# Kernel optimization log

Hardware: AMD Instinct MI355X
Metric: run time of the kernel (lower is better)

Reference implementation:

```python
import jax, jax.numpy as jnp
import numpy as np

# Grid derived from voxel_size=[0.2,0.2,0.2], pcr=[0,-40,-3,70.4,40,1]
NX, NY, NZ, NB = 352, 400, 20, 4


def setup_inputs() -> dict:
    key = jax.random.key(0)
    N, C = 1_000_000, 64
    kp, kb, kz, ky, kx = jax.random.split(key, 5)
    points = jax.random.normal(kp, (N, C), dtype=jnp.float32)
    b = jax.random.randint(kb, (N,), 0, NB)
    z = jax.random.randint(kz, (N,), 0, NZ)
    y = jax.random.randint(ky, (N,), 0, NY)
    x = jax.random.randint(kx, (N,), 0, NX)
    coors = jnp.stack([b, z, y, x], axis=1).astype(jnp.int32)
    return {"points": points, "coors": coors}


def reference(points, coors):
    # Dynamic scatter with mean reduction (average_points=True):
    # group points sharing the same (batch, z, y, x) voxel coordinate and
    # average their features. Padded (unused) voxel slots have coor == -1
    # and zero features, so the output shape is static ([N, C]).
    N = points.shape[0]
    b, z, y, x = coors[:, 0], coors[:, 1], coors[:, 2], coors[:, 3]
    keys = ((b.astype(jnp.int64) * NZ + z) * NY + y) * NX + x  # linearized voxel id

    uniq, inv = jnp.unique(keys, return_inverse=True, size=N, fill_value=-1)
    inv = inv.reshape(-1)

    sums = jax.ops.segment_sum(points, inv, num_segments=N)          # [N, C]
    counts = jax.ops.segment_sum(jnp.ones((N,), points.dtype), inv, num_segments=N)
    voxels = sums / jnp.maximum(counts, 1.0)[:, None]

    # decode linearized keys back to (batch, z, y, x); -1 marks padding
    valid = uniq >= 0
    ux = uniq % NX
    uy = (uniq // NX) % NY
    uz = (uniq // (NX * NY)) % NZ
    ub = uniq // (NX * NY * NZ)
    voxel_coors = jnp.stack([ub, uz, uy, ux], axis=1).astype(jnp.int32)
    voxel_coors = jnp.where(valid[:, None], voxel_coors, -1)
    return voxels, voxel_coors
```

## Files before the change

kernel.cpp:

```cpp
#include <hip/hip_runtime.h>
#include <stdint.h>

#define NXc 352
#define NYc 400
#define NZc 20
#define KS  11264000
#define WORDS 176000
#define NBLK3 688
#define NCH 64
#define RPT 4

#define OFF_A     0ull
#define OFF_P     11264000ull
#define OFF_R     12672000ull
#define OFF_BP    13376000ull
#define OFF_BC    13380096ull
#define OFF_NU    13384192ull
#define OFF_KEY   13384448ull
#define OFF_IOFF  17384448ull
#define OFF_PID   21384704ull

static __device__ __forceinline__ int keyof(int4 c) {
  return ((c.x * NZc + c.y) * NYc + c.z) * NXc + c.w;
}

__global__ void k_zero(uint4* __restrict__ A4, unsigned int m) {
  unsigned int i = blockIdx.x * 256 + threadIdx.x;
  unsigned int stride = gridDim.x * 256;
  uint4 z = make_uint4(0u, 0u, 0u, 0u);
  for (; i < m; i += stride) A4[i] = z;
}

__global__ void k_count(const int4* __restrict__ coors, unsigned int* __restrict__ A32, int n) {
  int p = blockIdx.x * 256 + threadIdx.x;
  if (p >= n) return;
  int key = keyof(coors[p]);
  atomicAdd(&A32[key >> 2], 1u << (8 * (key & 3)));
}

__global__ void k_scan1(const unsigned char* __restrict__ A,
                        unsigned int* __restrict__ bp, unsigned int* __restrict__ bc) {
  int b = blockIdx.x, t = threadIdx.x;
  int w = b * 256 + t;
  unsigned int pres = 0, cnt = 0;
  if (w < WORDS) {
    const uint4* aw = (const uint4*)(A + (size_t)w * 64);
    unsigned long long mask = 0ull;
#pragma unroll
    for (int q = 0; q < 4; q++) {
      uint4 v = aw[q];
      unsigned int us[4] = { v.x, v.y, v.z, v.w };
#pragma unroll
      for (int i = 0; i < 4; i++) {
        unsigned int u = us[i];
#pragma unroll
        for (int bb = 0; bb < 4; bb++) {
          unsigned int byte = (u >> (8 * bb)) & 0xFFu;
          cnt += byte;
          if (byte) mask |= 1ull << (q * 16 + i * 4 + bb);
        }
      }
    }
    pres = (unsigned int)__popcll(mask);
  }
  __shared__ unsigned int sp[256], sc[256];
  sp[t] = pres; sc[t] = cnt; __syncthreads();
  for (int o = 128; o > 0; o >>= 1) {
    if (t < o) { sp[t] += sp[t + o]; sc[t] += sc[t + o]; }
    __syncthreads();
  }
  if (t == 0) { bp[b] = sp[0]; bc[b] = sc[0]; }
}

__global__ void k_scan2(unsigned int* __restrict__ bp, unsigned int* __restrict__ bc,
                        unsigned int* __restrict__ nu, unsigned int* __restrict__ ioff, int n) {
  int t = threadIdx.x;
  __shared__ unsigned int sp[256], sc[256];
  unsigned int cp = 0, cc = 0;
  for (int base = 0; base < NBLK3; base += 256) {
    int i = base + t;
    unsigned int vp = (i < NBLK3) ? bp[i] : 0u;
    unsigned int vc = (i < NBLK3) ? bc[i] : 0u;
    sp[t] = vp; sc[t] = vc; __syncthreads();
    unsigned int ipv = vp, icv = vc;
    for (int o = 1; o < 256; o <<= 1) {
      unsigned int ap = (t >= o) ? sp[t - o] : 0u;
      unsigned int ac = (t >= o) ? sc[t - o] : 0u;
      __syncthreads();
      ipv += ap; icv += ac;
      sp[t] = ipv; sc[t] = icv; __syncthreads();
    }
    if (i < NBLK3) { bp[i] = cp + ipv - vp; bc[i] = cc + icv - vc; }
    unsigned int tp = sp[255], tc = sc[255];
    __syncthreads();
    cp += tp; cc += tc;
  }
  if (t == 0) { nu[0] = cp; ioff[cp] = (unsigned int)n; }
}

__global__ void k_scan3(const unsigned char* __restrict__ A,
                        const unsigned int* __restrict__ bp, const unsigned int* __restrict__ bc,
                        unsigned long long* __restrict__ P, unsigned int* __restrict__ R,
                        unsigned int* __restrict__ keyA, unsigned int* __restrict__ ioff) {
  int b = blockIdx.x, t = threadIdx.x;
  int w = b * 256 + t;
  unsigned long long mask = 0ull;
  unsigned int uu[16];
  unsigned int pres = 0, cnt = 0;
  if (w < WORDS) {
    const uint4* aw = (const uint4*)(A + (size_t)w * 64);
#pragma unroll
    for (int q = 0; q < 4; q++) {
      uint4 v = aw[q];
      uu[q * 4 + 0] = v.x; uu[q * 4 + 1] = v.y; uu[q * 4 + 2] = v.z; uu[q * 4 + 3] = v.w;
    }
#pragma unroll
    for (int i = 0; i < 16; i++) {
      unsigned int u = uu[i];
#pragma unroll
      for (int bb = 0; bb < 4; bb++) {
        unsigned int byte = (u >> (8 * bb)) & 0xFFu;
        cnt += byte;
        if (byte) mask |= 1ull << (i * 4 + bb);
      }
    }
    pres = (unsigned int)__popcll(mask);
  }
  __shared__ unsigned int sp[256], sc[256];
  sp[t] = pres; sc[t] = cnt; __syncthreads();
  unsigned int ip = pres, ic = cnt;
  for (int o = 1; o < 256; o <<= 1) {
    unsigned int ap = (t >= o) ? sp[t - o] : 0u;
    unsigned int ac = (t >= o) ? sc[t - o] : 0u;
    __syncthreads();
    ip += ap; ic += ac;
    sp[t] = ip; sc[t] = ic; __syncthreads();
  }
  if (w < WORDS) {
    unsigned int rank = bp[b] + ip - pres;
    unsigned int coff = bc[b] + ic - cnt;
    P[w] = mask; R[w] = rank;
    for (int j = 0; j < 64; j++) {
      unsigned int byte = (uu[j >> 2] >> (8 * (j & 3))) & 0xFFu;
      if (byte) {
        keyA[rank] = (unsigned int)(w * 64 + j);
        ioff[rank] = coff;
        rank++; coff += byte;
      }
    }
  }
}

__global__ void k_scatter(const int4* __restrict__ coors, unsigned int* __restrict__ A32,
                          const unsigned long long* __restrict__ P, const unsigned int* __restrict__ R,
                          const unsigned int* __restrict__ ioff, unsigned int* __restrict__ pid, int n) {
  int p = blockIdx.x * 256 + threadIdx.x;
  if (p >= n) return;
  int key = keyof(coors[p]);
  int w = key >> 6, bit = key & 63;
  unsigned long long below = (bit == 0) ? 0ull : (P[w] & ((1ull << bit) - 1ull));
  unsigned int rank = R[w] + (unsigned int)__popcll(below);
  unsigned int sh = 8u * (unsigned int)(key & 3);
  unsigned int old = atomicSub(&A32[key >> 2], 1u << sh);
  unsigned int intra = ((old >> sh) & 0xFFu) - 1u;
  pid[ioff[rank] + intra] = (unsigned int)p;
}

__global__ void k_gather(const float4* __restrict__ pts, const unsigned int* __restrict__ pid,
                         const unsigned int* __restrict__ keyA, const unsigned int* __restrict__ ioff,
                         const unsigned int* __restrict__ nu, float* __restrict__ out, int n) {
  int gt = blockIdx.x * 256 + threadIdx.x;
  int grp = gt >> 4, l = gt & 15;
  int rb = grp * RPT;
  if (rb >= n) return;
  unsigned int nU = nu[0];

  unsigned int e[RPT + 1];
#pragma unroll
  for (int j = 0; j <= RPT; j++) {
    unsigned int idx = min((unsigned int)(rb + j), nU);
    e[j] = ioff[idx];
  }

  unsigned int p0[RPT];
#pragma unroll
  for (int j = 0; j < RPT; j++)
    p0[j] = (e[j] < e[j + 1]) ? pid[e[j]] : 0u;

  float4 acc[RPT];
#pragma unroll
  for (int j = 0; j < RPT; j++) {
    if (e[j] < e[j + 1]) acc[j] = pts[(size_t)p0[j] * 16 + l];
    else                 acc[j] = make_float4(0.f, 0.f, 0.f, 0.f);
  }

#pragma unroll
  for (int j = 0; j < RPT; j++) {
    unsigned int span = e[j + 1] - e[j];
    for (unsigned int i = e[j] + 1; i < e[j + 1]; i++) {
      unsigned int p = pid[i];
      float4 v = pts[(size_t)p * 16 + l];
      acc[j].x += v.x; acc[j].y += v.y; acc[j].z += v.z; acc[j].w += v.w;
    }
    if (span > 1) {
      float inv = 1.0f / (float)span;
      acc[j].x *= inv; acc[j].y *= inv; acc[j].z *= inv; acc[j].w *= inv;
    }
  }

#pragma unroll
  for (int j = 0; j < RPT; j++) {
    int r = rb + j;
    if (r < n) ((float4*)out)[(size_t)r * 16 + l] = acc[j];
  }
  if (l == 0) {
#pragma unroll
    for (int j = 0; j < RPT; j++) {
      int r = rb + j;
      if (r >= n) break;
      float* oc = out + (size_t)n * NCH + (size_t)r * 4;
      float4 cc4;
      if ((unsigned int)r < nU) {
        unsigned int k = keyA[r];
        unsigned int x = k % NXc; unsigned int k2 = k / NXc;
        unsigned int y = k2 % NYc; unsigned int k3 = k2 / NYc;
        unsigned int z = k3 % NZc; unsigned int bb = k3 / NZc;
        cc4 = make_float4((float)bb, (float)z, (float)y, (float)x);
      } else {
        cc4 = make_float4(-1.f, -1.f, -1.f, -1.f);
      }
      *((float4*)oc) = cc4;
    }
  }
}

extern "C" void kernel_launch(void* const* d_in, const int* in_sizes, int n_in,
                              void* d_out, int out_size, void* d_ws, size_t ws_size,
                              hipStream_t stream) {
  const float4* pts = (const float4*)d_in[0];
  const int4* coors = (const int4*)d_in[1];
  int n = in_sizes[1] / 4;
  float* out = (float*)d_out;
  char* ws = (char*)d_ws;
  unsigned char*      A    = (unsigned char*)(ws + OFF_A);
  unsigned int*       A32  = (unsigned int*)(ws + OFF_A);
  unsigned long long* P    = (unsigned long long*)(ws + OFF_P);
  unsigned int*       R    = (unsigned int*)(ws + OFF_R);
  unsigned int*       bp   = (unsigned int*)(ws + OFF_BP);
  unsigned int*       bc   = (unsigned int*)(ws + OFF_BC);
  unsigned int*       nu   = (unsigned int*)(ws + OFF_NU);
  unsigned int*       keyA = (unsigned int*)(ws + OFF_KEY);
  unsigned int*       ioff = (unsigned int*)(ws + OFF_IOFF);
  unsigned int*       pid  = (unsigned int*)(ws + OFF_PID);

  k_zero   <<<2048,  256, 0, stream>>>((uint4*)A, (unsigned int)(KS / 16));
  int nb = (n + 255) / 256;
  k_count  <<<nb,    256, 0, stream>>>(coors, A32, n);
  k_scan1  <<<NBLK3, 256, 0, stream>>>(A, bp, bc);
  k_scan2  <<<1,     256, 0, stream>>>(bp, bc, nu, ioff, n);
  k_scan3  <<<NBLK3, 256, 0, stream>>>(A, bp, bc, P, R, keyA, ioff);
  k_scatter<<<nb,    256, 0, stream>>>(coors, A32, P, R, ioff, pid, n);
  int ngrp = (n + RPT - 1) / RPT;
  int gb = (ngrp * 16 + 255) / 256;
  k_gather <<<gb,    256, 0, stream>>>(pts, pid, keyA, ioff, nu, out, n);
}
```

Baseline: 237.2 us.

## Fuse three-pass scan into single-pass decoupled look-back scan and move coord decode

Replaces the three scan kernels (block reduce, single-block scan, rescan) with one single-pass decoupled look-back scan using packed status descriptors. This saves a full re-read of the 11 MB count array and two kernel launches. Voxel coordinate decoding and the -1 padding fill move out of the gather kernel into the scan and zero kernels. Per-point keys are cached in k_count so scatter does not recompute them, and rows per thread group in gather rise from 4 to 8. The look-back relies on forward progress of earlier blocks, which can deadlock if blocks are not scheduled in order.

```diff
diff --git a/kernel.cpp b/kernel.cpp
--- a/kernel.cpp
+++ b/kernel.cpp
@@ -6,102 +6,52 @@
 #define NZc 20
 #define KS  11264000
 #define WORDS 176000
-#define NBLK3 688
+#define NBLKS 688
 #define NCH 64
-#define RPT 4
+#define RPT 8
 
 #define OFF_A     0ull
 #define OFF_P     11264000ull
 #define OFF_R     12672000ull
-#define OFF_BP    13376000ull
-#define OFF_BC    13380096ull
-#define OFF_NU    13384192ull
-#define OFF_KEY   13384448ull
-#define OFF_IOFF  17384448ull
-#define OFF_PID   21384704ull
+#define OFF_DESC  13376000ull
+#define OFF_NU    13381504ull
+#define OFF_KEYPT 13381760ull
+#define OFF_IOFF  17381760ull
+#define OFF_PID   21381760ull
 
 static __device__ __forceinline__ int keyof(int4 c) {
   return ((c.x * NZc + c.y) * NYc + c.z) * NXc + c.w;
 }
 
-__global__ void k_zero(uint4* __restrict__ A4, unsigned int m) {
-  unsigned int i = blockIdx.x * 256 + threadIdx.x;
-  unsigned int stride = gridDim.x * 256;
+static __device__ __forceinline__ unsigned long long packd(unsigned int st, unsigned int p, unsigned int c) {
+  return ((unsigned long long)st << 62) | ((unsigned long long)p << 31) | (unsigned long long)c;
+}
+
+__global__ void k_zero(uint4* __restrict__ A4, unsigned int mA,
+                       uint4* __restrict__ D4, unsigned int mD,
+                       float4* __restrict__ C4, unsigned int mC) {
+  unsigned int i = blockIdx.x * 256 + threadIdx.x, s = gridDim.x * 256;
   uint4 z = make_uint4(0u, 0u, 0u, 0u);
-  for (; i < m; i += stride) A4[i] = z;
-}
-
-__global__ void k_count(const int4* __restrict__ coors, unsigned int* __restrict__ A32, int n) {
+  for (unsigned int j = i; j < mA; j += s) A4[j] = z;
+  for (unsigned int j = i; j < mD; j += s) D4[j] = z;
+  float4 m1 = make_float4(-1.f, -1.f, -1.f, -1.f);
+  for (unsigned int j = i; j < mC; j += s) C4[j] = m1;
+}
+
+__global__ void k_count(const int4* __restrict__ coors, unsigned int* __restrict__ A32,
+                        int* __restrict__ keyPt, int n) {
   int p = blockIdx.x * 256 + threadIdx.x;
   if (p >= n) return;
   int key = keyof(coors[p]);
+  keyPt[p] = key;
   atomicAdd(&A32[key >> 2], 1u << (8 * (key & 3)));
 }
 
-__global__ void k_scan1(const unsigned char* __restrict__ A,
-                        unsigned int* __restrict__ bp, unsigned int* __restrict__ bc) {
-  int b = blockIdx.x, t = threadIdx.x;
-  int w = b * 256 + t;
-  unsigned int pres = 0, cnt = 0;
-  if (w < WORDS) {
-    const uint4* aw = (const uint4*)(A + (size_t)w * 64);
-    unsigned long long mask = 0ull;
-#pragma unroll
-    for (int q = 0; q < 4; q++) {
-      uint4 v = aw[q];
-      unsigned int us[4] = { v.x, v.y, v.z, v.w };
-#pragma unroll
-      for (int i = 0; i < 4; i++) {
-        unsigned int u = us[i];
-#pragma unroll
-        for (int bb = 0; bb < 4; bb++) {
-          unsigned int byte = (u >> (8 * bb)) & 0xFFu;
-          cnt += byte;
-          if (byte) mask |= 1ull << (q * 16 + i * 4 + bb);
-        }
-      }
-    }
-    pres = (unsigned int)__popcll(mask);
-  }
-  __shared__ unsigned int sp[256], sc[256];
-  sp[t] = pres; sc[t] = cnt; __syncthreads();
-  for (int o = 128; o > 0; o >>= 1) {
-    if (t < o) { sp[t] += sp[t + o]; sc[t] += sc[t + o]; }
-    __syncthreads();
-  }
-  if (t == 0) { bp[b] = sp[0]; bc[b] = sc[0]; }
-}
-
-__global__ void k_scan2(unsigned int* __restrict__ bp, unsigned int* __restrict__ bc,
-                        unsigned int* __restrict__ nu, unsigned int* __restrict__ ioff, int n) {
-  int t = threadIdx.x;
-  __shared__ unsigned int sp[256], sc[256];
-  unsigned int cp = 0, cc = 0;
-  for (int base = 0; base < NBLK3; base += 256) {
-    int i = base + t;
-    unsigned int vp = (i < NBLK3) ? bp[i] : 0u;
-    unsigned int vc = (i < NBLK3) ? bc[i] : 0u;
-    sp[t] = vp; sc[t] = vc; __syncthreads();
-    unsigned int ipv = vp, icv = vc;
-    for (int o = 1; o < 256; o <<= 1) {
-      unsigned int ap = (t >= o) ? sp[t - o] : 0u;
-      unsigned int ac = (t >= o) ? sc[t - o] : 0u;
-      __syncthreads();
-      ipv += ap; icv += ac;
-      sp[t] = ipv; sc[t] = icv; __syncthreads();
-    }
-    if (i < NBLK3) { bp[i] = cp + ipv - vp; bc[i] = cc + icv - vc; }
-    unsigned int tp = sp[255], tc = sc[255];
-    __syncthreads();
-    cp += tp; cc += tc;
-  }
-  if (t == 0) { nu[0] = cp; ioff[cp] = (unsigned int)n; }
-}
-
-__global__ void k_scan3(const unsigned char* __restrict__ A,
-                        const unsigned int* __restrict__ bp, const unsigned int* __restrict__ bc,
-                        unsigned long long* __restrict__ P, unsigned int* __restrict__ R,
-                        unsigned int* __restrict__ keyA, unsigned int* __restrict__ ioff) {
+__global__ void k_scan(const unsigned char* __restrict__ A,
+                       unsigned long long* __restrict__ desc,
+                       unsigned long long* __restrict__ P, unsigned int* __restrict__ R,
+                       unsigned int* __restrict__ ioff, unsigned int* __restrict__ nu,
+                       float4* __restrict__ outc, int n) {
   int b = blockIdx.x, t = threadIdx.x;
   int w = b * 256 + t;
   unsigned long long mask = 0ull;
@@ -136,30 +86,62 @@
     ip += ap; ic += ac;
     sp[t] = ip; sc[t] = ic; __syncthreads();
   }
+  __shared__ unsigned int exc2[2];
+  if (t == 0) {
+    unsigned int aggP = sp[255], aggC = sc[255];
+    unsigned int eP = 0, eC = 0;
+    if (b == 0) {
+      atomicExch(&desc[0], packd(2u, aggP, aggC));
+    } else {
+      atomicExch(&desc[b], packd(1u, aggP, aggC));
+      int j = b - 1;
+      for (;;) {
+        unsigned long long d = atomicAdd(&desc[j], 0ull);
+        unsigned int st = (unsigned int)(d >> 62);
+        if (st == 0u) continue;
+        eP += (unsigned int)((d >> 31) & 0x7FFFFFFFull);
+        eC += (unsigned int)(d & 0x7FFFFFFFull);
+        if (st == 2u) break;
+        --j;
+      }
+      atomicExch(&desc[b], packd(2u, eP + aggP, eC + aggC));
+    }
+    exc2[0] = eP; exc2[1] = eC;
+    if (b == NBLKS - 1) {
+      unsigned int tot = eP + aggP;
+      nu[0] = tot;
+      ioff[tot] = (unsigned int)n;
+    }
+  }
+  __syncthreads();
+  unsigned int excP = exc2[0], excC = exc2[1];
   if (w < WORDS) {
-    unsigned int rank = bp[b] + ip - pres;
-    unsigned int coff = bc[b] + ic - cnt;
+    unsigned int rank = excP + ip - pres;
+    unsigned int coff = excC + ic - cnt;
     P[w] = mask; R[w] = rank;
     for (int j = 0; j < 64; j++) {
       unsigned int byte = (uu[j >> 2] >> (8 * (j & 3))) & 0xFFu;
       if (byte) {
-        keyA[rank] = (unsigned int)(w * 64 + j);
         ioff[rank] = coff;
+        unsigned int k = (unsigned int)w * 64u + (unsigned int)j;
+        unsigned int x = k % NXc; unsigned int k2 = k / NXc;
+        unsigned int y = k2 % NYc; unsigned int k3 = k2 / NYc;
+        unsigned int z = k3 % NZc; unsigned int bb = k3 / NZc;
+        outc[rank] = make_float4((float)bb, (float)z, (float)y, (float)x);
         rank++; coff += byte;
       }
     }
   }
 }
 
-__global__ void k_scatter(const int4* __restrict__ coors, unsigned int* __restrict__ A32,
+__global__ void k_scatter(const int* __restrict__ keyPt, unsigned int* __restrict__ A32,
                           const unsigned long long* __restrict__ P, const unsigned int* __restrict__ R,
                           const unsigned int* __restrict__ ioff, unsigned int* __restrict__ pid, int n) {
   int p = blockIdx.x * 256 + threadIdx.x;
   if (p >= n) return;
-  int key = keyof(coors[p]);
+  int key = keyPt[p];
   int w = key >> 6, bit = key & 63;
-  unsigned long long below = (bit == 0) ? 0ull : (P[w] & ((1ull << bit) - 1ull));
-  unsigned int rank = R[w] + (unsigned int)__popcll(below);
+  unsigned int rank = R[w] + (unsigned int)__popcll(P[w] & ((1ull << bit) - 1ull));
   unsigned int sh = 8u * (unsigned int)(key & 3);
   unsigned int old = atomicSub(&A32[key >> 2], 1u << sh);
   unsigned int intra = ((old >> sh) & 0xFFu) - 1u;
@@ -167,8 +149,8 @@
 }
 
 __global__ void k_gather(const float4* __restrict__ pts, const unsigned int* __restrict__ pid,
-                         const unsigned int* __restrict__ keyA, const unsigned int* __restrict__ ioff,
-                         const unsigned int* __restrict__ nu, float* __restrict__ out, int n) {
+                         const unsigned int* __restrict__ ioff, const unsigned int* __restrict__ nu,
+                         float* __restrict__ out, int n) {
   int gt = blockIdx.x * 256 + threadIdx.x;
   int grp = gt >> 4, l = gt & 15;
   int rb = grp * RPT;
@@ -212,25 +194,6 @@
   for (int j = 0; j < RPT; j++) {
     int r = rb + j;
     if (r < n) ((float4*)out)[(size_t)r * 16 + l] = acc[j];
-  }
-  if (l == 0) {
-#pragma unroll
-    for (int j = 0; j < RPT; j++) {
-      int r = rb + j;
-      if (r >= n) break;
-      float* oc = out + (size_t)n * NCH + (size_t)r * 4;
-      float4 cc4;
-      if ((unsigned int)r < nU) {
-        unsigned int k = keyA[r];
-        unsigned int x = k % NXc; unsigned int k2 = k / NXc;
-        unsigned int y = k2 % NYc; unsigned int k3 = k2 / NYc;
-        unsigned int z = k3 % NZc; unsigned int bb = k3 / NZc;
-        cc4 = make_float4((float)bb, (float)z, (float)y, (float)x);
-      } else {
-        cc4 = make_float4(-1.f, -1.f, -1.f, -1.f);
-      }
-      *((float4*)oc) = cc4;
-    }
   }
 }
 
@@ -246,21 +209,21 @@
   unsigned int*       A32  = (unsigned int*)(ws + OFF_A);
   unsigned long long* P    = (unsigned long long*)(ws + OFF_P);
   unsigned int*       R    = (unsigned int*)(ws + OFF_R);
-  unsigned int*       bp   = (unsigned int*)(ws + OFF_BP);
-  unsigned int*       bc   = (unsigned int*)(ws + OFF_BC);
+  unsigned long long* desc = (unsigned long long*)(ws + OFF_DESC);
   unsigned int*       nu   = (unsigned int*)(ws + OFF_NU);
-  unsigned int*       keyA = (unsigned int*)(ws + OFF_KEY);
+  int*                keyPt= (int*)(ws + OFF_KEYPT);
   unsigned int*       ioff = (unsigned int*)(ws + OFF_IOFF);
   unsigned int*       pid  = (unsigned int*)(ws + OFF_PID);
-
-  k_zero   <<<2048,  256, 0, stream>>>((uint4*)A, (unsigned int)(KS / 16));
+  float4*             outc = (float4*)(out + (size_t)n * NCH);
+
+  k_zero   <<<2048,  256, 0, stream>>>((uint4*)A, (unsigned int)(KS / 16),
+                                       (uint4*)desc, (unsigned int)(NBLKS * 8 / 16),
+                                       outc, (unsigned int)n);
   int nb = (n + 255) / 256;
-  k_count  <<<nb,    256, 0, stream>>>(coors, A32, n);
-  k_scan1  <<<NBLK3, 256, 0, stream>>>(A, bp, bc);
-  k_scan2  <<<1,     256, 0, stream>>>(bp, bc, nu, ioff, n);
-  k_scan3  <<<NBLK3, 256, 0, stream>>>(A, bp, bc, P, R, keyA, ioff);
-  k_scatter<<<nb,    256, 0, stream>>>(coors, A32, P, R, ioff, pid, n);
+  k_count  <<<nb,    256, 0, stream>>>(coors, A32, keyPt, n);
+  k_scan   <<<NBLKS, 256, 0, stream>>>(A, desc, P, R, ioff, nu, outc, n);
+  k_scatter<<<nb,    256, 0, stream>>>(keyPt, A32, P, R, ioff, pid, n);
   int ngrp = (n + RPT - 1) / RPT;
   int gb = (ngrp * 16 + 255) / 256;
-  k_gather <<<gb,    256, 0, stream>>>(pts, pid, keyA, ioff, nu, out, n);
-}
+  k_gather <<<gb,    256, 0, stream>>>(pts, pid, ioff, nu, out, n);
+}
```

New measurement: 237.6 us. No clear change (+0.2%).
